# Optimization experiments

Hardware: AMD Instinct MI355X
Metric: run time of the kernel (lower is better)

## Reference

```python
import jax, jax.numpy as jnp
import numpy as np

EMBED_DIM = 256
NUM_HEADS = 8
TEMPERATURE = 10000.0
SCALE = 100.0
EPS = 1e-5


def setup_inputs() -> dict:
    key = jax.random.key(0)
    k1, k2, k3 = jax.random.split(key, 3)
    B, N, H, Wd = 1, 300, 24, 80
    # depths in a realistic positive range
    predict_depth = jax.random.uniform(k1, (B, N), dtype=jnp.float32) * 60.0
    depth_map = jax.random.uniform(k2, (B, H, Wd), dtype=jnp.float32) * 60.0
    # nn.Linear(embed_dim, num_heads): store as (in, out)
    W = jax.random.normal(k3, (EMBED_DIM, NUM_HEADS), dtype=jnp.float32) * 0.05
    b = jnp.zeros((NUM_HEADS,), dtype=jnp.float32)
    return {"predict_depth": predict_depth, "depth_map": depth_map, "W": W, "b": b}


def reference(predict_depth, depth_map, W, b):
    B, H, Wd = depth_map.shape
    HW = H * Wd
    N = predict_depth.shape[1]
    dm = depth_map.reshape(B, HW)
    pd = jax.nn.relu(predict_depth)
    # depth log-ratio: (B, N, HW)
    delta = jnp.log((pd[:, :, None] + EPS) / (dm[:, None, :] + EPS))
    # sine/cos embedding with interleaved sin/cos per frequency -> (B, N, HW, 256)
    dim_t = TEMPERATURE ** (jnp.arange(EMBED_DIM // 2, dtype=jnp.float32) * 2.0 / EMBED_DIM)
    pos = delta[..., None] * SCALE / dim_t  # (B, N, HW, 128)
    pos = jnp.stack((jnp.sin(pos), jnp.cos(pos)), axis=-1).reshape(B, N, HW, EMBED_DIM)
    # computed under torch.no_grad() in the original
    pos = jax.lax.stop_gradient(pos)
    # Linear(256 -> num_heads) + ReLU
    out = jax.nn.relu(pos @ W + b)  # (B, N, HW, heads)
    # permute(0,3,1,2).flatten(0,1) -> (B*heads, N, HW)
    out = jnp.transpose(out, (0, 3, 1, 2)).reshape(B * NUM_HEADS, N, HW)
    return out
```

## Files before the change

kernel.cpp:

```cpp
#include <hip/hip_runtime.h>
#include <hip/hip_bf16.h>

#define NPTS   300
#define HW_SZ  1920
#define NH     8
#define TOTAL  (NPTS * HW_SZ)
#define NCOL   2400
#define L2T128 0.10381025293350249f

#define BM  64
#define BN  64
#define LDK 72
#define SNP 129
#define WLP 17
#define MT  (HW_SZ / BM)
#define CT  38

typedef __attribute__((ext_vector_type(8))) short short8;
typedef __attribute__((ext_vector_type(4))) float floatx4;

__device__ __forceinline__ unsigned bf16_rne(float x) {
    unsigned u = __float_as_uint(x);
    return (u + 0x7fffu + ((u >> 16) & 1u)) >> 16;
}

__global__ __launch_bounds__(256, 4) void dre_fused3(const float* __restrict__ pd,
                                                     const float* __restrict__ dm,
                                                     const float* __restrict__ W,
                                                     const float* __restrict__ b,
                                                     float* __restrict__ out)
{
    __shared__ float kf[128];
    __shared__ float ldm[BM];
    __shared__ float sn[8 * SNP];
    __shared__ float cn[8 * SNP];
    __shared__ float wl[128 * WLP];
    __shared__ unsigned short As[BM * LDK];
    __shared__ unsigned short Bs[BN * LDK];

    const int tid = threadIdx.x;
    const int m0  = blockIdx.x * BM;
    const int c0  = blockIdx.y * BN;
    const int n0  = c0 >> 3;

    if (tid < 128)      kf[tid] = 100.0f * exp2f(-(float)tid * L2T128);
    else if (tid < 192) ldm[tid - 128] = __logf(dm[m0 + tid - 128] + 1e-5f);
    {
        const int i = tid >> 1, half = tid & 1;
#pragma unroll
        for (int j = 0; j < 8; ++j)
            wl[i * WLP + half * 8 + j] = W[i * 16 + half * 8 + j];
    }
    __syncthreads();

    {
        const int nl = tid >> 5;
        const int nn = n0 + nl;
        const float pv = (nn < NPTS) ? pd[nn] : 0.0f;
        const float lp = __logf(fmaxf(pv, 0.0f) + 1e-5f);
#pragma unroll
        for (int j = 0; j < 4; ++j) {
            const int i = (tid & 31) * 4 + j;
            float s, c;
            __sincosf(kf[i] * lp, &s, &c);
            sn[nl * SNP + i] = s;
            cn[nl * SNP + i] = c;
        }
    }

    const int w    = tid >> 6;
    const int lane = tid & 63;
    const int quad = lane >> 4;
    const int l16  = lane & 15;

    const int arow = tid >> 2;
    const int akb  = (tid & 3) * 16;
    const int bcr  = tid >> 2;
    const int bkb  = (tid & 3) * 16;
    const int bnl  = bcr >> 3;
    const int bh   = bcr & 7;

    floatx4 acc[4];
#pragma unroll
    for (int nf = 0; nf < 4; ++nf) acc[nf] = (floatx4){0.f, 0.f, 0.f, 0.f};

    unsigned stash[2][8];

    __syncthreads();
    const float ld = ldm[arow];

#pragma unroll
    for (int ch = 0; ch < 4; ++ch) {
        const int ibase = (ch & 1) * 64;
        if (ch < 2) {
            unsigned uc[8];
#pragma unroll
            for (int g = 0; g < 8; ++g) {
                const int i = ibase + akb + 2 * g;
                float s0, c0v, s1, c1v;
                __sincosf(kf[i] * ld,     &s0, &c0v);
                __sincosf(kf[i + 1] * ld, &s1, &c1v);
                uc[g]        = bf16_rne(c0v) | (bf16_rne(c1v) << 16);
                stash[ch][g] = bf16_rne(s0)  | (bf16_rne(s1)  << 16);
            }
            *(uint4*)&As[arow * LDK + akb]     = make_uint4(uc[0], uc[1], uc[2], uc[3]);
            *(uint4*)&As[arow * LDK + akb + 8] = make_uint4(uc[4], uc[5], uc[6], uc[7]);
        } else {
            const unsigned* st = stash[ch - 2];
            *(uint4*)&As[arow * LDK + akb]     = make_uint4(st[0], st[1], st[2], st[3]);
            *(uint4*)&As[arow * LDK + akb + 8] = make_uint4(st[4], st[5], st[6], st[7]);
        }
        {
            unsigned uq[8];
#pragma unroll
            for (int g = 0; g < 8; ++g) {
                const int i = ibase + bkb + 2 * g;
                const float s0  = sn[bnl * SNP + i],     cc0 = cn[bnl * SNP + i];
                const float s1  = sn[bnl * SNP + i + 1], cc1 = cn[bnl * SNP + i + 1];
                const float ws0 = wl[i * WLP + bh],       wc0 = wl[i * WLP + 8 + bh];
                const float ws1 = wl[(i+1) * WLP + bh],   wc1 = wl[(i+1) * WLP + 8 + bh];
                float v0, v1;
                if (ch < 2) { v0 = ws0*s0 + wc0*cc0; v1 = ws1*s1 + wc1*cc1; }
                else        { v0 = wc0*s0 - ws0*cc0; v1 = wc1*s1 - ws1*cc1; }
                uq[g] = bf16_rne(v0) | (bf16_rne(v1) << 16);
            }
            *(uint4*)&Bs[bcr * LDK + bkb]     = make_uint4(uq[0], uq[1], uq[2], uq[3]);
            *(uint4*)&Bs[bcr * LDK + bkb + 8] = make_uint4(uq[4], uq[5], uq[6], uq[7]);
        }
        __syncthreads();

#pragma unroll
        for (int ks = 0; ks < 2; ++ks) {
            const int koff = ks * 32 + quad * 8;
            short8 a0 = *(const short8*)(&As[(w * 16 + l16) * LDK + koff]);
#pragma unroll
            for (int nf = 0; nf < 4; ++nf) {
                short8 bb = *(const short8*)(&Bs[(nf * 16 + l16) * LDK + koff]);
                acc[nf] = __builtin_amdgcn_mfma_f32_16x16x32_bf16(a0, bb, acc[nf], 0, 0, 0);
            }
        }
        __syncthreads();
    }

    const float bias = b[lane & 7];
#pragma unroll
    for (int nf = 0; nf < 4; ++nf) {
        const int c = c0 + nf * 16 + l16;
        if (c < NCOL) {
            const int n = c >> 3, h = c & 7;
            const int hw = m0 + w * 16 + quad * 4;
            floatx4 v = acc[nf];
            v.x = fmaxf(v.x + bias, 0.0f);
            v.y = fmaxf(v.y + bias, 0.0f);
            v.z = fmaxf(v.z + bias, 0.0f);
            v.w = fmaxf(v.w + bias, 0.0f);
            *(floatx4*)(out + (size_t)h * TOTAL + (size_t)n * HW_SZ + hw) = v;
        }
    }
}

extern "C" void kernel_launch(void* const* d_in, const int* in_sizes, int n_in,
                              void* d_out, int out_size, void* d_ws, size_t ws_size,
                              hipStream_t stream) {
    const float* pd = (const float*)d_in[0];
    const float* dm = (const float*)d_in[1];
    const float* W  = (const float*)d_in[2];
    const float* b  = (const float*)d_in[3];
    float* out = (float*)d_out;

    dre_fused3<<<dim3(MT, CT), 256, 0, stream>>>(pd, dm, W, b, out);
}
```

Measured before the change: 81.38 us.

## Build A fragments in MFMA registers, double-buffer B tile, transpose W in LDS

The A operand (cos/sin of the depth-map term) is now computed directly in each lane's MFMA register layout, with sin values stashed for the later chunks. This removes the As shared tile and its LDS round trip. The B tile is double-buffered, so the trailing barrier in each chunk is dropped. W is stored transposed in LDS so four values load with one float4. Float-to-bf16 packing now uses a single perm with round-half-up instead of the exact round-to-nearest-even sequence, which slightly changes rounding behaviour.

```diff
diff --git a/kernel.cpp b/kernel.cpp
--- a/kernel.cpp
+++ b/kernel.cpp
@@ -3,7 +3,6 @@
 
 #define NPTS   300
 #define HW_SZ  1920
-#define NH     8
 #define TOTAL  (NPTS * HW_SZ)
 #define NCOL   2400
 #define L2T128 0.10381025293350249f
@@ -11,48 +10,51 @@
 #define BM  64
 #define BN  64
 #define LDK 72
-#define SNP 129
-#define WLP 17
-#define MT  (HW_SZ / BM)
+#define SNP 132
+#define WTP 132
+#define MT  30
 #define CT  38
 
 typedef __attribute__((ext_vector_type(8))) short short8;
 typedef __attribute__((ext_vector_type(4))) float floatx4;
 
-__device__ __forceinline__ unsigned bf16_rne(float x) {
-    unsigned u = __float_as_uint(x);
-    return (u + 0x7fffu + ((u >> 16) & 1u)) >> 16;
+union frag_u { unsigned u[4]; short8 s; };
+
+__device__ __forceinline__ unsigned pk_bf16(float lo, float hi) {
+    return __builtin_amdgcn_perm(__float_as_uint(hi) + 0x8000u,
+                                 __float_as_uint(lo) + 0x8000u,
+                                 0x07060302u);
 }
 
-__global__ __launch_bounds__(256, 4) void dre_fused3(const float* __restrict__ pd,
-                                                     const float* __restrict__ dm,
-                                                     const float* __restrict__ W,
-                                                     const float* __restrict__ b,
-                                                     float* __restrict__ out)
+__global__ __launch_bounds__(256, 4) void dre_v10(const float* __restrict__ pd,
+                                                  const float* __restrict__ dm,
+                                                  const float* __restrict__ W,
+                                                  const float* __restrict__ b,
+                                                  float* __restrict__ out)
 {
-    __shared__ float kf[128];
+    __shared__ float kfr[128];
     __shared__ float ldm[BM];
-    __shared__ float sn[8 * SNP];
-    __shared__ float cn[8 * SNP];
-    __shared__ float wl[128 * WLP];
-    __shared__ unsigned short As[BM * LDK];
-    __shared__ unsigned short Bs[BN * LDK];
+    __shared__ float snq[8 * SNP];
+    __shared__ float cnq[8 * SNP];
+    __shared__ float wst[8 * WTP];
+    __shared__ float wct[8 * WTP];
+    __shared__ unsigned short Bs[2][BN * LDK];
 
     const int tid = threadIdx.x;
     const int m0  = blockIdx.x * BM;
     const int c0  = blockIdx.y * BN;
     const int n0  = c0 >> 3;
 
-    if (tid < 128)      kf[tid] = 100.0f * exp2f(-(float)tid * L2T128);
+    if (tid < 128)      kfr[tid] = 100.0f * exp2f(-(float)tid * L2T128);
     else if (tid < 192) ldm[tid - 128] = __logf(dm[m0 + tid - 128] + 1e-5f);
-    {
-        const int i = tid >> 1, half = tid & 1;
 #pragma unroll
-        for (int j = 0; j < 8; ++j)
-            wl[i * WLP + half * 8 + j] = W[i * 16 + half * 8 + j];
+    for (int v = 0; v < 8; ++v) {
+        const int lin = tid * 8 + v;
+        const int arr = lin >> 10, rest = lin & 1023;
+        const int h = rest >> 7, i = rest & 127;
+        const float val = W[i * 16 + arr * 8 + h];
+        (arr ? wct : wst)[h * WTP + i] = val;
     }
-    __syncthreads();
-
     {
         const int nl = tid >> 5;
         const int nn = n0 + nl;
@@ -61,85 +63,96 @@
 #pragma unroll
         for (int j = 0; j < 4; ++j) {
             const int i = (tid & 31) * 4 + j;
+            const float k = 100.0f * exp2f(-(float)i * L2T128);
             float s, c;
-            __sincosf(kf[i] * lp, &s, &c);
-            sn[nl * SNP + i] = s;
-            cn[nl * SNP + i] = c;
+            __sincosf(k * lp, &s, &c);
+            snq[nl * SNP + i] = s;
+            cnq[nl * SNP + i] = c;
         }
     }
 
-    const int w    = tid >> 6;
-    const int lane = tid & 63;
-    const int quad = lane >> 4;
-    const int l16  = lane & 15;
-
-    const int arow = tid >> 2;
-    const int akb  = (tid & 3) * 16;
-    const int bcr  = tid >> 2;
-    const int bkb  = (tid & 3) * 16;
-    const int bnl  = bcr >> 3;
-    const int bh   = bcr & 7;
+    const int w = tid >> 6, lane = tid & 63, quad = lane >> 4, l16 = lane & 15;
+    const int bcr = tid >> 2, q = tid & 3;
+    const int bnl = bcr >> 3, bh = bcr & 7;
 
     floatx4 acc[4];
 #pragma unroll
     for (int nf = 0; nf < 4; ++nf) acc[nf] = (floatx4){0.f, 0.f, 0.f, 0.f};
 
-    unsigned stash[2][8];
+    unsigned astash[2][2][4];
+    unsigned qstash[2][8];
 
     __syncthreads();
-    const float ld = ldm[arow];
+    const float ld_row = ldm[w * 16 + l16];
 
 #pragma unroll
     for (int ch = 0; ch < 4; ++ch) {
         const int ibase = (ch & 1) * 64;
+        unsigned short* bsb = Bs[ch & 1];
+        frag_u af[2];
+
         if (ch < 2) {
-            unsigned uc[8];
+            unsigned pp[8];
 #pragma unroll
-            for (int g = 0; g < 8; ++g) {
-                const int i = ibase + akb + 2 * g;
-                float s0, c0v, s1, c1v;
-                __sincosf(kf[i] * ld,     &s0, &c0v);
-                __sincosf(kf[i + 1] * ld, &s1, &c1v);
-                uc[g]        = bf16_rne(c0v) | (bf16_rne(c1v) << 16);
-                stash[ch][g] = bf16_rne(s0)  | (bf16_rne(s1)  << 16);
+            for (int g = 0; g < 4; ++g) {
+                const int i4 = ibase + q * 16 + g * 4;
+                const float4 s4 = *(const float4*)&snq[bnl * SNP + i4];
+                const float4 c4 = *(const float4*)&cnq[bnl * SNP + i4];
+                const float4 a4 = *(const float4*)&wst[bh * WTP + i4];
+                const float4 o4 = *(const float4*)&wct[bh * WTP + i4];
+                const float P0 = a4.x*s4.x + o4.x*c4.x, P1 = a4.y*s4.y + o4.y*c4.y;
+                const float P2 = a4.z*s4.z + o4.z*c4.z, P3 = a4.w*s4.w + o4.w*c4.w;
+                const float Q0 = o4.x*s4.x - a4.x*c4.x, Q1 = o4.y*s4.y - a4.y*c4.y;
+                const float Q2 = o4.z*s4.z - a4.z*c4.z, Q3 = o4.w*s4.w - a4.w*c4.w;
+                pp[2*g]   = pk_bf16(P0, P1);
+                pp[2*g+1] = pk_bf16(P2, P3);
+                qstash[ch][2*g]   = pk_bf16(Q0, Q1);
+                qstash[ch][2*g+1] = pk_bf16(Q2, Q3);
             }
-            *(uint4*)&As[arow * LDK + akb]     = make_uint4(uc[0], uc[1], uc[2], uc[3]);
-            *(uint4*)&As[arow * LDK + akb + 8] = make_uint4(uc[4], uc[5], uc[6], uc[7]);
+            *(uint4*)&bsb[bcr * LDK + q * 16]     = make_uint4(pp[0], pp[1], pp[2], pp[3]);
+            *(uint4*)&bsb[bcr * LDK + q * 16 + 8] = make_uint4(pp[4], pp[5], pp[6], pp[7]);
+
+#pragma unroll
+            for (int ks = 0; ks < 2; ++ks) {
+                const int kb = ibase + ks * 32 + quad * 8;
+                const float4 f0 = *(const float4*)&kfr[kb];
+                const float4 f1 = *(const float4*)&kfr[kb + 4];
+                float s[8], c[8];
+                __sincosf(f0.x * ld_row, &s[0], &c[0]);
+                __sincosf(f0.y * ld_row, &s[1], &c[1]);
+                __sincosf(f0.z * ld_row, &s[2], &c[2]);
+                __sincosf(f0.w * ld_row, &s[3], &c[3]);
+                __sincosf(f1.x * ld_row, &s[4], &c[4]);
+                __sincosf(f1.y * ld_row, &s[5], &c[5]);
+                __sincosf(f1.z * ld_row, &s[6], &c[6]);
+                __sincosf(f1.w * ld_row, &s[7], &c[7]);
+#pragma unroll
+                for (int r = 0; r < 4; ++r) {
+                    af[ks].u[r]          = pk_bf16(c[2*r], c[2*r+1]);
+                    astash[ch][ks][r]    = pk_bf16(s[2*r], s[2*r+1]);
+                }
+            }
         } else {
-            const unsigned* st = stash[ch - 2];
-            *(uint4*)&As[arow * LDK + akb]     = make_uint4(st[0], st[1], st[2], st[3]);
-            *(uint4*)&As[arow * LDK + akb + 8] = make_uint4(st[4], st[5], st[6], st[7]);
+            const unsigned* qs = qstash[ch - 2];
+            *(uint4*)&bsb[bcr * LDK + q * 16]     = make_uint4(qs[0], qs[1], qs[2], qs[3]);
+            *(uint4*)&bsb[bcr * LDK + q * 16 + 8] = make_uint4(qs[4], qs[5], qs[6], qs[7]);
+#pragma unroll
+            for (int ks = 0; ks < 2; ++ks)
+#pragma unroll
+                for (int r = 0; r < 4; ++r) af[ks].u[r] = astash[ch - 2][ks][r];
         }
-        {
-            unsigned uq[8];
-#pragma unroll
-            for (int g = 0; g < 8; ++g) {
-                const int i = ibase + bkb + 2 * g;
-                const float s0  = sn[bnl * SNP + i],     cc0 = cn[bnl * SNP + i];
-                const float s1  = sn[bnl * SNP + i + 1], cc1 = cn[bnl * SNP + i + 1];
-                const float ws0 = wl[i * WLP + bh],       wc0 = wl[i * WLP + 8 + bh];
-                const float ws1 = wl[(i+1) * WLP + bh],   wc1 = wl[(i+1) * WLP + 8 + bh];
-                float v0, v1;
-                if (ch < 2) { v0 = ws0*s0 + wc0*cc0; v1 = ws1*s1 + wc1*cc1; }
-                else        { v0 = wc0*s0 - ws0*cc0; v1 = wc1*s1 - ws1*cc1; }
-                uq[g] = bf16_rne(v0) | (bf16_rne(v1) << 16);
-            }
-            *(uint4*)&Bs[bcr * LDK + bkb]     = make_uint4(uq[0], uq[1], uq[2], uq[3]);
-            *(uint4*)&Bs[bcr * LDK + bkb + 8] = make_uint4(uq[4], uq[5], uq[6], uq[7]);
-        }
+
         __syncthreads();
 
 #pragma unroll
         for (int ks = 0; ks < 2; ++ks) {
             const int koff = ks * 32 + quad * 8;
-            short8 a0 = *(const short8*)(&As[(w * 16 + l16) * LDK + koff]);
 #pragma unroll
             for (int nf = 0; nf < 4; ++nf) {
-                short8 bb = *(const short8*)(&Bs[(nf * 16 + l16) * LDK + koff]);
-                acc[nf] = __builtin_amdgcn_mfma_f32_16x16x32_bf16(a0, bb, acc[nf], 0, 0, 0);
+                short8 bb = *(const short8*)&bsb[(nf * 16 + l16) * LDK + koff];
+                acc[nf] = __builtin_amdgcn_mfma_f32_16x16x32_bf16(af[ks].s, bb, acc[nf], 0, 0, 0);
             }
         }
-        __syncthreads();
     }
 
     const float bias = b[lane & 7];
@@ -168,5 +181,5 @@
     const float* b  = (const float*)d_in[3];
     float* out = (float*)d_out;
 
-    dre_fused3<<<dim3(MT, CT), 256, 0, stream>>>(pd, dm, W, b, out);
+    dre_v10<<<dim3(MT, CT), 256, 0, stream>>>(pd, dm, W, b, out);
 }
```

New measurement: 78.08 us. 4.0% less time.
